# Kernel optimization log

Hardware: AMD Instinct MI355X
Metric: run time of the kernel (lower is better)

## Reference

```python
import jax, jax.numpy as jnp
import numpy as np

NEG = -1000000.0  # mask fill value used by the torch module


def setup_inputs() -> dict:
    key = jax.random.key(0)
    k1, k2, k3, k4 = jax.random.split(key, 4)
    B, L, D = 64, 1024, 64
    return {
        "queries": jax.random.normal(k1, (B, L, D), dtype=jnp.float32),
        "keys": jax.random.normal(k2, (B, L, D), dtype=jnp.float32),
        "values": jax.random.normal(k3, (B, L, D), dtype=jnp.float32),
        "valid_lens": jax.random.randint(k4, (B,), 1, 1024, dtype=jnp.int32),
    }


def reference(queries, keys, values, valid_lens):
    d = queries.shape[-1]
    # [B, Lq, Lk] attention scores
    scores = jnp.einsum("bqd,bkd->bqk", queries, keys) / jnp.sqrt(jnp.asarray(d, queries.dtype))
    Lk = scores.shape[-1]
    # sequence mask: key positions >= valid_len are filled with NEG (per batch)
    col = jnp.arange(Lk)  # [Lk]
    mask = col[None, None, :] >= valid_lens[:, None, None]  # [B, 1, Lk] -> broadcasts over q
    scores = jnp.where(mask, NEG, scores)
    attn = jax.nn.softmax(scores, axis=-1)
    # dropout p=0.0 (eval) -> identity
    return jnp.einsum("bqk,bkd->bqd", attn, values)
```

## Files before the change

### kernel.cpp

```cpp
#include <hip/hip_runtime.h>
#include <math.h>


typedef __attribute__((ext_vector_type(4))) float f32x4;
typedef __attribute__((ext_vector_type(8))) short bf16x8;
typedef __attribute__((ext_vector_type(8))) unsigned short u16x8;

constexpr int Bn = 64, Ln = 1024, Dn = 64;
constexpr float QSCALE = 0.125f * 1.44269504088896340736f;
constexpr float DEFER_THR = 10.0f;

__device__ inline unsigned short f2bf(float x) {
    unsigned int u = __float_as_uint(x);
    return (unsigned short)((u + 0x7fffu + ((u >> 16) & 1u)) >> 16);
}

__global__ __launch_bounds__(256) void flash_attn(
    const float* __restrict__ Q, const float* __restrict__ K,
    const float* __restrict__ V, const int* __restrict__ VL,
    float* __restrict__ O)
{
    __shared__ unsigned short kls[64 * 64];
    __shared__ unsigned short vls[64 * 64];
    __shared__ unsigned short plds[4][16 * 64];

    const int tid = threadIdx.x;
    const int w = tid >> 6, l = tid & 63;
    const int lg = l >> 4, ln = l & 15;
    const int b = blockIdx.x >> 4;
    const int qt = blockIdx.x & 15;
    const int qbase = qt * 64 + w * 16;
    const int valid = VL[b];
    const int nkt = (valid + 63) >> 6;

    const float* Kbase = K + (size_t)b * Ln * Dn;
    const float* Vbase = V + (size_t)b * Ln * Dn;

    bf16x8 aq0, aq1;
    {
        const f32x4* qp = reinterpret_cast<const f32x4*>(Q + ((size_t)b * Ln + qbase + ln) * Dn);
        f32x4 q0 = qp[lg * 2], q1 = qp[lg * 2 + 1], q2 = qp[8 + lg * 2], q3 = qp[8 + lg * 2 + 1];
        #pragma unroll
        for (int j = 0; j < 4; ++j) {
            aq0[j]     = (short)f2bf(q0[j] * QSCALE);
            aq0[j + 4] = (short)f2bf(q1[j] * QSCALE);
            aq1[j]     = (short)f2bf(q2[j] * QSCALE);
            aq1[j + 4] = (short)f2bf(q3[j] * QSCALE);
        }
    }

    const int kr = tid >> 2, kc = (tid & 3) * 16;
    const int vd = l, vk0 = w * 16;

    f32x4 kpre[4];
    float vpre[16];
    {
        const f32x4* kp = reinterpret_cast<const f32x4*>(Kbase + (size_t)kr * Dn + kc);
        #pragma unroll
        for (int i = 0; i < 4; ++i) kpre[i] = kp[i];
        const float* vp = Vbase + (size_t)vk0 * Dn + vd;
        #pragma unroll
        for (int i = 0; i < 16; ++i) vpre[i] = vp[(size_t)i * Dn];
    }

    f32x4 acc[4] = {{0.f,0.f,0.f,0.f},{0.f,0.f,0.f,0.f},{0.f,0.f,0.f,0.f},{0.f,0.f,0.f,0.f}};
    float mrow[4] = {-1e30f, -1e30f, -1e30f, -1e30f};
    float lrow[4] = {0.f, 0.f, 0.f, 0.f};
    unsigned short* pw = plds[w];
    char* klsb = reinterpret_cast<char*>(kls);
    char* vlsb = reinterpret_cast<char*>(vls);
    char* pwb  = reinterpret_cast<char*>(pw);

    for (int kt = 0; kt < nkt; ++kt) {
        __syncthreads();
        {
            u16x8 c0, c1;
            #pragma unroll
            for (int j = 0; j < 4; ++j) {
                c0[j]     = f2bf(kpre[0][j]);  c0[j + 4] = f2bf(kpre[1][j]);
                c1[j]     = f2bf(kpre[2][j]);  c1[j + 4] = f2bf(kpre[3][j]);
            }
            const int kb = kr * 128 + kc * 2, ksw = (kr & 7) << 4;
            *reinterpret_cast<u16x8*>(klsb + ((kb)      ^ ksw)) = c0;
            *reinterpret_cast<u16x8*>(klsb + ((kb + 16) ^ ksw)) = c1;
            u16x8 v0, v1;
            #pragma unroll
            for (int j = 0; j < 8; ++j) { v0[j] = f2bf(vpre[j]); v1[j] = f2bf(vpre[j + 8]); }
            const int vb = vd * 128 + vk0 * 2, vsw = (vd & 7) << 4;
            *reinterpret_cast<u16x8*>(vlsb + ((vb)      ^ vsw)) = v0;
            *reinterpret_cast<u16x8*>(vlsb + ((vb + 16) ^ vsw)) = v1;
        }
        __syncthreads();

        if (kt + 1 < nkt) {
            const f32x4* kp = reinterpret_cast<const f32x4*>(Kbase + (size_t)((kt + 1) * 64 + kr) * Dn + kc);
            #pragma unroll
            for (int i = 0; i < 4; ++i) kpre[i] = kp[i];
            const float* vp = Vbase + (size_t)((kt + 1) * 64 + vk0) * Dn + vd;
            #pragma unroll
            for (int i = 0; i < 16; ++i) vpre[i] = vp[(size_t)i * Dn];
        }

        f32x4 st[4] = {{0.f,0.f,0.f,0.f},{0.f,0.f,0.f,0.f},{0.f,0.f,0.f,0.f},{0.f,0.f,0.f,0.f}};
        #pragma unroll
        for (int t = 0; t < 4; ++t) {
            const int r = 16 * t + ln, rsw = (r & 7) << 4;
            bf16x8 bk0 = *reinterpret_cast<const bf16x8*>(klsb + ((r * 128 + lg * 16)      ^ rsw));
            st[t] = __builtin_amdgcn_mfma_f32_16x16x32_bf16(aq0, bk0, st[t], 0, 0, 0);
            bf16x8 bk1 = *reinterpret_cast<const bf16x8*>(klsb + ((r * 128 + lg * 16 + 64) ^ rsw));
            st[t] = __builtin_amdgcn_mfma_f32_16x16x32_bf16(aq1, bk1, st[t], 0, 0, 0);
        }

        const int kbase = kt * 64;
        if (kbase + 64 > valid) {
            #pragma unroll
            for (int t = 0; t < 4; ++t) {
                const bool msk = (kbase + 16 * t + ln) >= valid;
                #pragma unroll
                for (int j = 0; j < 4; ++j) if (msk) st[t][j] = -1e30f;
            }
        }

        float mx[4];
        #pragma unroll
        for (int j = 0; j < 4; ++j) {
            float m0 = fmaxf(fmaxf(st[0][j], st[1][j]), fmaxf(st[2][j], st[3][j]));
            #pragma unroll
            for (int off = 8; off >= 1; off >>= 1) m0 = fmaxf(m0, __shfl_xor(m0, off, 64));
            mx[j] = m0;
        }
        const float g = fmaxf(fmaxf(mx[0] - mrow[0], mx[1] - mrow[1]),
                              fmaxf(mx[2] - mrow[2], mx[3] - mrow[3]));
        if (__any(g > DEFER_THR)) {
            #pragma unroll
            for (int j = 0; j < 4; ++j) {
                const float mn = fmaxf(mrow[j], mx[j]);
                const float rs = exp2f(mrow[j] - mn);
                mrow[j] = mn;
                lrow[j] *= rs;
                #pragma unroll
                for (int t = 0; t < 4; ++t) acc[t][j] *= rs;
            }
        }
        #pragma unroll
        for (int j = 0; j < 4; ++j) {
            const int q = lg * 4 + j, qsw = (q & 7) << 4;
            float rs = 0.f;
            #pragma unroll
            for (int t = 0; t < 4; ++t) {
                const float p = exp2f(st[t][j] - mrow[j]);
                rs += p;
                const int col = 16 * t + ln;
                *reinterpret_cast<unsigned short*>(pwb + ((q * 128 + col * 2) ^ qsw)) = f2bf(p);
            }
            #pragma unroll
            for (int off = 8; off >= 1; off >>= 1) rs += __shfl_xor(rs, off, 64);
            lrow[j] += rs;
        }

        #pragma unroll
        for (int s = 0; s < 2; ++s) {
            bf16x8 pa = *reinterpret_cast<const bf16x8*>(
                pwb + ((ln * 128 + lg * 16 + 64 * s) ^ ((ln & 7) << 4)));
            #pragma unroll
            for (int t = 0; t < 4; ++t) {
                const int r = 16 * t + ln, rsw = (r & 7) << 4;
                bf16x8 bv = *reinterpret_cast<const bf16x8*>(vlsb + ((r * 128 + lg * 16 + 64 * s) ^ rsw));
                acc[t] = __builtin_amdgcn_mfma_f32_16x16x32_bf16(pa, bv, acc[t], 0, 0, 0);
            }
        }
    }

    float inv[4];
    #pragma unroll
    for (int j = 0; j < 4; ++j) inv[j] = 1.0f / lrow[j];
    float* Orow = O + ((size_t)b * Ln + qbase) * Dn;
    #pragma unroll
    for (int t = 0; t < 4; ++t) {
        #pragma unroll
        for (int j = 0; j < 4; ++j) {
            const int q = lg * 4 + j;
            const int d = 16 * t + ln;
            Orow[(size_t)q * Dn + d] = acc[t][j] * inv[j];
        }
    }
}

extern "C" void kernel_launch(void* const* d_in, const int* in_sizes, int n_in,
                              void* d_out, int out_size, void* d_ws, size_t ws_size,
                              hipStream_t stream) {
    const float* Q = (const float*)d_in[0];
    const float* K = (const float*)d_in[1];
    const float* V = (const float*)d_in[2];
    const int* VL = (const int*)d_in[3];
    float* O = (float*)d_out;
    flash_attn<<<Bn * 16, 256, 0, stream>>>(Q, K, V, VL, O);
}
```

Measured before the change: 137.7 us.

## Split KV range across blocks (split-K flash attention) with a reduction kernel

Divides each query tile's key range into up to four chunks processed by separate blocks, writing unnormalized partial accumulators plus the row max and sum to workspace, then a second kernel combines them with log-sum-exp rescaling. The aim is more parallelism and better load balance, since valid lengths vary per batch and the long sequences previously serialized inside one block. The cost is extra workspace traffic (up to four times the output size written and read back in fp32) and a second launch, and the path only runs if the harness provides enough workspace.

```diff
diff --git a/kernel.cpp b/kernel.cpp
--- a/kernel.cpp
+++ b/kernel.cpp
@@ -7,6 +7,7 @@
 typedef __attribute__((ext_vector_type(8))) unsigned short u16x8;
 
 constexpr int Bn = 64, Ln = 1024, Dn = 64;
+constexpr int NROW = Bn * Ln;
 constexpr float QSCALE = 0.125f * 1.44269504088896340736f;
 constexpr float DEFER_THR = 10.0f;
 
@@ -18,7 +19,7 @@
 __global__ __launch_bounds__(256) void flash_attn(
     const float* __restrict__ Q, const float* __restrict__ K,
     const float* __restrict__ V, const int* __restrict__ VL,
-    float* __restrict__ O)
+    float* __restrict__ O, float* __restrict__ ws, int S)
 {
     __shared__ unsigned short kls[64 * 64];
     __shared__ unsigned short vls[64 * 64];
@@ -27,11 +28,19 @@
     const int tid = threadIdx.x;
     const int w = tid >> 6, l = tid & 63;
     const int lg = l >> 4, ln = l & 15;
-    const int b = blockIdx.x >> 4;
-    const int qt = blockIdx.x & 15;
+    const int blk = blockIdx.x;
+    const int c = blk % S;
+    const int bq = blk / S;
+    const int b = bq >> 4;
+    const int qt = bq & 15;
     const int qbase = qt * 64 + w * 16;
     const int valid = VL[b];
-    const int nkt = (valid + 63) >> 6;
+
+    const int nkt_total = (valid + 63) >> 6;
+    const int tpc = 16 / S;
+    const int t0 = c * tpc;
+    const int t1 = min(nkt_total, t0 + tpc);
+    if (t0 >= t1) return;
 
     const float* Kbase = K + (size_t)b * Ln * Dn;
     const float* Vbase = V + (size_t)b * Ln * Dn;
@@ -55,10 +64,10 @@
     f32x4 kpre[4];
     float vpre[16];
     {
-        const f32x4* kp = reinterpret_cast<const f32x4*>(Kbase + (size_t)kr * Dn + kc);
+        const f32x4* kp = reinterpret_cast<const f32x4*>(Kbase + (size_t)(t0 * 64 + kr) * Dn + kc);
         #pragma unroll
         for (int i = 0; i < 4; ++i) kpre[i] = kp[i];
-        const float* vp = Vbase + (size_t)vk0 * Dn + vd;
+        const float* vp = Vbase + (size_t)(t0 * 64 + vk0) * Dn + vd;
         #pragma unroll
         for (int i = 0; i < 16; ++i) vpre[i] = vp[(size_t)i * Dn];
     }
@@ -71,7 +80,7 @@
     char* vlsb = reinterpret_cast<char*>(vls);
     char* pwb  = reinterpret_cast<char*>(pw);
 
-    for (int kt = 0; kt < nkt; ++kt) {
+    for (int kt = t0; kt < t1; ++kt) {
         __syncthreads();
         {
             u16x8 c0, c1;
@@ -92,7 +101,7 @@
         }
         __syncthreads();
 
-        if (kt + 1 < nkt) {
+        if (kt + 1 < t1) {
             const f32x4* kp = reinterpret_cast<const f32x4*>(Kbase + (size_t)((kt + 1) * 64 + kr) * Dn + kc);
             #pragma unroll
             for (int i = 0; i < 4; ++i) kpre[i] = kp[i];
@@ -171,19 +180,69 @@
         }
     }
 
-    float inv[4];
-    #pragma unroll
-    for (int j = 0; j < 4; ++j) inv[j] = 1.0f / lrow[j];
-    float* Orow = O + ((size_t)b * Ln + qbase) * Dn;
-    #pragma unroll
-    for (int t = 0; t < 4; ++t) {
-        #pragma unroll
-        for (int j = 0; j < 4; ++j) {
-            const int q = lg * 4 + j;
-            const int d = 16 * t + ln;
-            Orow[(size_t)q * Dn + d] = acc[t][j] * inv[j];
-        }
-    }
+    if (S == 1) {
+        float inv[4];
+        #pragma unroll
+        for (int j = 0; j < 4; ++j) inv[j] = 1.0f / lrow[j];
+        float* Orow = O + ((size_t)b * Ln + qbase) * Dn;
+        #pragma unroll
+        for (int t = 0; t < 4; ++t) {
+            #pragma unroll
+            for (int j = 0; j < 4; ++j) {
+                const int q = lg * 4 + j;
+                const int d = 16 * t + ln;
+                Orow[(size_t)q * Dn + d] = acc[t][j] * inv[j];
+            }
+        }
+    } else {
+        float* accb = ws;
+        float* mb = ws + (size_t)S * NROW * Dn;
+        float* lb = mb + (size_t)S * NROW;
+        const int rowbase = b * Ln + qbase;
+        #pragma unroll
+        for (int t = 0; t < 4; ++t) {
+            #pragma unroll
+            for (int j = 0; j < 4; ++j) {
+                const int row = rowbase + lg * 4 + j;
+                const int d = 16 * t + ln;
+                accb[((size_t)c * NROW + row) * Dn + d] = acc[t][j];
+            }
+        }
+        if (ln == 0) {
+            #pragma unroll
+            for (int j = 0; j < 4; ++j) {
+                const int row = rowbase + lg * 4 + j;
+                mb[(size_t)c * NROW + row] = mrow[j];
+                lb[(size_t)c * NROW + row] = lrow[j];
+            }
+        }
+    }
+}
+
+__global__ __launch_bounds__(256) void reduce_k(
+    const float* __restrict__ ws, const int* __restrict__ VL,
+    float* __restrict__ O, int S)
+{
+    const int gid = blockIdx.x * 256 + threadIdx.x;
+    const int r = gid >> 6, d = gid & 63;
+    const int b = r >> 10;
+    const int valid = VL[b];
+    const int CH = Ln / S;
+    const int nc = min(S, (valid + CH - 1) / CH);
+
+    const float* accb = ws;
+    const float* mb = ws + (size_t)S * NROW * Dn;
+    const float* lb = mb + (size_t)S * NROW;
+
+    float m = -1e30f;
+    for (int c = 0; c < nc; ++c) m = fmaxf(m, mb[(size_t)c * NROW + r]);
+    float o = 0.f, L = 0.f;
+    for (int c = 0; c < nc; ++c) {
+        const float e = exp2f(mb[(size_t)c * NROW + r] - m);
+        o += accb[((size_t)c * NROW + r) * Dn + d] * e;
+        L += lb[(size_t)c * NROW + r] * e;
+    }
+    O[(size_t)r * Dn + d] = o / L;
 }
 
 extern "C" void kernel_launch(void* const* d_in, const int* in_sizes, int n_in,
@@ -194,5 +253,14 @@
     const float* V = (const float*)d_in[2];
     const int* VL = (const int*)d_in[3];
     float* O = (float*)d_out;
-    flash_attn<<<Bn * 16, 256, 0, stream>>>(Q, K, V, VL, O);
-}
+    float* ws = (float*)d_ws;
+
+    const size_t per_chunk = ((size_t)NROW * Dn + 2 * (size_t)NROW) * sizeof(float);
+    int S = 1;
+    if (ws_size >= 4 * per_chunk) S = 4;
+    else if (ws_size >= 2 * per_chunk) S = 2;
+
+    flash_attn<<<Bn * 16 * S, 256, 0, stream>>>(Q, K, V, VL, O, ws, S);
+    if (S > 1)
+        reduce_k<<<NROW * Dn / 256, 256, 0, stream>>>(ws, VL, O, S);
+}
```

Result: slower. 175.4 us (+27.3%).

## Double-buffer K/V LDS tiles and transpose QK^T MFMA for per-lane row softmax

Applied to the files above, without the earlier changes.

K and V shared-memory tiles are now double-buffered, so the next tile is written after the PV MFMAs and only one barrier is needed per iteration instead of two. The QK^T MFMA operands are swapped so each lane holds scores for a single query row. This lets the row max and row sum use two cross-lane shuffles instead of four, and lets P be stored as packed 4-element vectors. The cost is double the K/V LDS footprint, which may reduce occupancy, plus extra shuffles to spread rescale factors across accumulator rows.

```diff
diff --git a/kernel.cpp b/kernel.cpp
--- a/kernel.cpp
+++ b/kernel.cpp
@@ -5,6 +5,7 @@
 typedef __attribute__((ext_vector_type(4))) float f32x4;
 typedef __attribute__((ext_vector_type(8))) short bf16x8;
 typedef __attribute__((ext_vector_type(8))) unsigned short u16x8;
+typedef __attribute__((ext_vector_type(4))) unsigned short u16x4;
 
 constexpr int Bn = 64, Ln = 1024, Dn = 64;
 constexpr float QSCALE = 0.125f * 1.44269504088896340736f;
@@ -20,8 +21,8 @@
     const float* __restrict__ V, const int* __restrict__ VL,
     float* __restrict__ O)
 {
-    __shared__ unsigned short kls[64 * 64];
-    __shared__ unsigned short vls[64 * 64];
+    __shared__ unsigned short kls[2][64 * 64];
+    __shared__ unsigned short vls[2][64 * 64];
     __shared__ unsigned short plds[4][16 * 64];
 
     const int tid = threadIdx.x;
@@ -36,16 +37,16 @@
     const float* Kbase = K + (size_t)b * Ln * Dn;
     const float* Vbase = V + (size_t)b * Ln * Dn;
 
-    bf16x8 aq0, aq1;
+    bf16x8 bq0, bq1;
     {
         const f32x4* qp = reinterpret_cast<const f32x4*>(Q + ((size_t)b * Ln + qbase + ln) * Dn);
         f32x4 q0 = qp[lg * 2], q1 = qp[lg * 2 + 1], q2 = qp[8 + lg * 2], q3 = qp[8 + lg * 2 + 1];
         #pragma unroll
         for (int j = 0; j < 4; ++j) {
-            aq0[j]     = (short)f2bf(q0[j] * QSCALE);
-            aq0[j + 4] = (short)f2bf(q1[j] * QSCALE);
-            aq1[j]     = (short)f2bf(q2[j] * QSCALE);
-            aq1[j + 4] = (short)f2bf(q3[j] * QSCALE);
+            bq0[j]     = (short)f2bf(q0[j] * QSCALE);
+            bq0[j + 4] = (short)f2bf(q1[j] * QSCALE);
+            bq1[j]     = (short)f2bf(q2[j] * QSCALE);
+            bq1[j + 4] = (short)f2bf(q3[j] * QSCALE);
         }
     }
 
@@ -54,6 +55,34 @@
 
     f32x4 kpre[4];
     float vpre[16];
+
+    char* const kls0 = reinterpret_cast<char*>(kls[0]);
+    char* const kls1 = reinterpret_cast<char*>(kls[1]);
+    char* const vls0 = reinterpret_cast<char*>(vls[0]);
+    char* const vls1 = reinterpret_cast<char*>(vls[1]);
+    char* const pwb  = reinterpret_cast<char*>(plds[w]);
+
+    const int kb = kr * 128 + kc * 2, ksw = (kr & 7) << 4;
+    const int vb = vd * 128 + vk0 * 2, vsw = (vd & 7) << 4;
+
+    auto stage_write = [&](int p) {
+        char* kd = p ? kls1 : kls0;
+        char* vd_ = p ? vls1 : vls0;
+        u16x8 c0, c1;
+        #pragma unroll
+        for (int j = 0; j < 4; ++j) {
+            c0[j]     = f2bf(kpre[0][j]);  c0[j + 4] = f2bf(kpre[1][j]);
+            c1[j]     = f2bf(kpre[2][j]);  c1[j + 4] = f2bf(kpre[3][j]);
+        }
+        *reinterpret_cast<u16x8*>(kd + ((kb)      ^ ksw)) = c0;
+        *reinterpret_cast<u16x8*>(kd + ((kb + 16) ^ ksw)) = c1;
+        u16x8 v0, v1;
+        #pragma unroll
+        for (int j = 0; j < 8; ++j) { v0[j] = f2bf(vpre[j]); v1[j] = f2bf(vpre[j + 8]); }
+        *reinterpret_cast<u16x8*>(vd_ + ((vb)      ^ vsw)) = v0;
+        *reinterpret_cast<u16x8*>(vd_ + ((vb + 16) ^ vsw)) = v1;
+    };
+
     {
         const f32x4* kp = reinterpret_cast<const f32x4*>(Kbase + (size_t)kr * Dn + kc);
         #pragma unroll
@@ -62,37 +91,20 @@
         #pragma unroll
         for (int i = 0; i < 16; ++i) vpre[i] = vp[(size_t)i * Dn];
     }
+    stage_write(0);
+    __syncthreads();
 
     f32x4 acc[4] = {{0.f,0.f,0.f,0.f},{0.f,0.f,0.f,0.f},{0.f,0.f,0.f,0.f},{0.f,0.f,0.f,0.f}};
-    float mrow[4] = {-1e30f, -1e30f, -1e30f, -1e30f};
-    float lrow[4] = {0.f, 0.f, 0.f, 0.f};
-    unsigned short* pw = plds[w];
-    char* klsb = reinterpret_cast<char*>(kls);
-    char* vlsb = reinterpret_cast<char*>(vls);
-    char* pwb  = reinterpret_cast<char*>(pw);
-
-    for (int kt = 0; kt < nkt; ++kt) {
-        __syncthreads();
-        {
-            u16x8 c0, c1;
-            #pragma unroll
-            for (int j = 0; j < 4; ++j) {
-                c0[j]     = f2bf(kpre[0][j]);  c0[j + 4] = f2bf(kpre[1][j]);
-                c1[j]     = f2bf(kpre[2][j]);  c1[j + 4] = f2bf(kpre[3][j]);
-            }
-            const int kb = kr * 128 + kc * 2, ksw = (kr & 7) << 4;
-            *reinterpret_cast<u16x8*>(klsb + ((kb)      ^ ksw)) = c0;
-            *reinterpret_cast<u16x8*>(klsb + ((kb + 16) ^ ksw)) = c1;
-            u16x8 v0, v1;
-            #pragma unroll
-            for (int j = 0; j < 8; ++j) { v0[j] = f2bf(vpre[j]); v1[j] = f2bf(vpre[j + 8]); }
-            const int vb = vd * 128 + vk0 * 2, vsw = (vd & 7) << 4;
-            *reinterpret_cast<u16x8*>(vlsb + ((vb)      ^ vsw)) = v0;
-            *reinterpret_cast<u16x8*>(vlsb + ((vb + 16) ^ vsw)) = v1;
-        }
-        __syncthreads();
-
-        if (kt + 1 < nkt) {
+    float mrow = -1e30f;
+    float lrow = 0.f;
+
+    int p = 0;
+    for (int kt = 0; kt < nkt; ++kt, p ^= 1) {
+        const bool has_next = (kt + 1 < nkt);
+        char* kcur = p ? kls1 : kls0;
+        char* vcur = p ? vls1 : vls0;
+
+        if (has_next) {
             const f32x4* kp = reinterpret_cast<const f32x4*>(Kbase + (size_t)((kt + 1) * 64 + kr) * Dn + kc);
             #pragma unroll
             for (int i = 0; i < 4; ++i) kpre[i] = kp[i];
@@ -105,75 +117,81 @@
         #pragma unroll
         for (int t = 0; t < 4; ++t) {
             const int r = 16 * t + ln, rsw = (r & 7) << 4;
-            bf16x8 bk0 = *reinterpret_cast<const bf16x8*>(klsb + ((r * 128 + lg * 16)      ^ rsw));
-            st[t] = __builtin_amdgcn_mfma_f32_16x16x32_bf16(aq0, bk0, st[t], 0, 0, 0);
-            bf16x8 bk1 = *reinterpret_cast<const bf16x8*>(klsb + ((r * 128 + lg * 16 + 64) ^ rsw));
-            st[t] = __builtin_amdgcn_mfma_f32_16x16x32_bf16(aq1, bk1, st[t], 0, 0, 0);
-        }
-
-        const int kbase = kt * 64;
-        if (kbase + 64 > valid) {
-            #pragma unroll
-            for (int t = 0; t < 4; ++t) {
-                const bool msk = (kbase + 16 * t + ln) >= valid;
+            bf16x8 ak0 = *reinterpret_cast<const bf16x8*>(kcur + ((r * 128 + lg * 16)      ^ rsw));
+            st[t] = __builtin_amdgcn_mfma_f32_16x16x32_bf16(ak0, bq0, st[t], 0, 0, 0);
+            bf16x8 ak1 = *reinterpret_cast<const bf16x8*>(kcur + ((r * 128 + lg * 16 + 64) ^ rsw));
+            st[t] = __builtin_amdgcn_mfma_f32_16x16x32_bf16(ak1, bq1, st[t], 0, 0, 0);
+        }
+
+        const int kb0 = kt * 64 + lg * 4;
+        if (kt * 64 + 64 > valid) {
+            #pragma unroll
+            for (int t = 0; t < 4; ++t)
                 #pragma unroll
-                for (int j = 0; j < 4; ++j) if (msk) st[t][j] = -1e30f;
+                for (int j = 0; j < 4; ++j)
+                    if (kb0 + 16 * t + j >= valid) st[t][j] = -1e30f;
+        }
+
+        float mx;
+        {
+            float a0 = fmaxf(fmaxf(st[0][0], st[0][1]), fmaxf(st[0][2], st[0][3]));
+            float a1 = fmaxf(fmaxf(st[1][0], st[1][1]), fmaxf(st[1][2], st[1][3]));
+            float a2 = fmaxf(fmaxf(st[2][0], st[2][1]), fmaxf(st[2][2], st[2][3]));
+            float a3 = fmaxf(fmaxf(st[3][0], st[3][1]), fmaxf(st[3][2], st[3][3]));
+            mx = fmaxf(fmaxf(a0, a1), fmaxf(a2, a3));
+            mx = fmaxf(mx, __shfl_xor(mx, 16, 64));
+            mx = fmaxf(mx, __shfl_xor(mx, 32, 64));
+        }
+
+        if (__any(mx - mrow > DEFER_THR)) {
+            const float mn = fmaxf(mrow, mx);
+            const float rs = exp2f(mrow - mn);
+            mrow = mn;
+            lrow *= rs;
+            #pragma unroll
+            for (int j = 0; j < 4; ++j) {
+                const float rsj = __shfl(rs, lg * 4 + j, 64);
+                #pragma unroll
+                for (int t = 0; t < 4; ++t) acc[t][j] *= rsj;
             }
         }
 
-        float mx[4];
-        #pragma unroll
-        for (int j = 0; j < 4; ++j) {
-            float m0 = fmaxf(fmaxf(st[0][j], st[1][j]), fmaxf(st[2][j], st[3][j]));
-            #pragma unroll
-            for (int off = 8; off >= 1; off >>= 1) m0 = fmaxf(m0, __shfl_xor(m0, off, 64));
-            mx[j] = m0;
-        }
-        const float g = fmaxf(fmaxf(mx[0] - mrow[0], mx[1] - mrow[1]),
-                              fmaxf(mx[2] - mrow[2], mx[3] - mrow[3]));
-        if (__any(g > DEFER_THR)) {
+        float rsum = 0.f;
+        const int psw = (ln & 7) << 4;
+        #pragma unroll
+        for (int t = 0; t < 4; ++t) {
+            u16x4 pk;
             #pragma unroll
             for (int j = 0; j < 4; ++j) {
-                const float mn = fmaxf(mrow[j], mx[j]);
-                const float rs = exp2f(mrow[j] - mn);
-                mrow[j] = mn;
-                lrow[j] *= rs;
-                #pragma unroll
-                for (int t = 0; t < 4; ++t) acc[t][j] *= rs;
+                const float pv = exp2f(st[t][j] - mrow);
+                rsum += pv;
+                pk[j] = f2bf(pv);
             }
-        }
-        #pragma unroll
-        for (int j = 0; j < 4; ++j) {
-            const int q = lg * 4 + j, qsw = (q & 7) << 4;
-            float rs = 0.f;
-            #pragma unroll
-            for (int t = 0; t < 4; ++t) {
-                const float p = exp2f(st[t][j] - mrow[j]);
-                rs += p;
-                const int col = 16 * t + ln;
-                *reinterpret_cast<unsigned short*>(pwb + ((q * 128 + col * 2) ^ qsw)) = f2bf(p);
-            }
-            #pragma unroll
-            for (int off = 8; off >= 1; off >>= 1) rs += __shfl_xor(rs, off, 64);
-            lrow[j] += rs;
-        }
+            *reinterpret_cast<u16x4*>(pwb + ((ln * 128 + 32 * t + 8 * lg) ^ psw)) = pk;
+        }
+        rsum += __shfl_xor(rsum, 16, 64);
+        rsum += __shfl_xor(rsum, 32, 64);
+        lrow += rsum;
 
         #pragma unroll
         for (int s = 0; s < 2; ++s) {
-            bf16x8 pa = *reinterpret_cast<const bf16x8*>(
-                pwb + ((ln * 128 + lg * 16 + 64 * s) ^ ((ln & 7) << 4)));
+            bf16x8 pa = *reinterpret_cast<const bf16x8*>(pwb + ((ln * 128 + lg * 16 + 64 * s) ^ psw));
             #pragma unroll
             for (int t = 0; t < 4; ++t) {
                 const int r = 16 * t + ln, rsw = (r & 7) << 4;
-                bf16x8 bv = *reinterpret_cast<const bf16x8*>(vlsb + ((r * 128 + lg * 16 + 64 * s) ^ rsw));
+                bf16x8 bv = *reinterpret_cast<const bf16x8*>(vcur + ((r * 128 + lg * 16 + 64 * s) ^ rsw));
                 acc[t] = __builtin_amdgcn_mfma_f32_16x16x32_bf16(pa, bv, acc[t], 0, 0, 0);
             }
         }
-    }
-
+
+        if (has_next) stage_write(p ^ 1);
+        __syncthreads();
+    }
+
+    const float invl = 1.0f / lrow;
     float inv[4];
     #pragma unroll
-    for (int j = 0; j < 4; ++j) inv[j] = 1.0f / lrow[j];
+    for (int j = 0; j < 4; ++j) inv[j] = __shfl(invl, lg * 4 + j, 64);
     float* Orow = O + ((size_t)b * Ln + qbase) * Dn;
     #pragma unroll
     for (int t = 0; t < 4; ++t) {
```

Measured after the change: 127.2 us. 7.6% less time.
